# Kernel optimization log

Hardware: AMD Instinct MI355X
Metric: run time of the kernel (lower is better)

## Reference

```python
import jax, jax.numpy as jnp
import numpy as np

B, N, K = 4, 8192, 16
FEAT = 512
GRID = 45
M = GRID * GRID


def _p(key, shape, scale=0.05):
    return jax.random.normal(key, shape, dtype=jnp.float32) * scale


def setup_inputs() -> dict:
    key = jax.random.key(0)
    ks = jax.random.split(key, 40)
    inp = {"pts": jax.random.normal(ks[0], (B, N, 3), dtype=jnp.float32)}
    specs = {
        "w1": (64, 12), "b1": (64,), "w2": (64, 64), "b2": (64,), "w3": (64, 64), "b3": (64,),
        "g1a": (64, 64), "g1ab": (64,), "g1b": (128, 64), "g1bb": (128,),
        "g2a": (128, 128), "g2ab": (128,), "g2b": (1024, 128), "g2bb": (1024,),
        "m1": (FEAT, 1024), "m1b": (FEAT,), "m2": (FEAT, FEAT), "m2b": (FEAT,),
        "f1a": (FEAT, FEAT + 2), "f1ab": (FEAT,), "f1b": (FEAT, FEAT), "f1bb": (FEAT,), "f1c": (3, FEAT), "f1cb": (3,),
        "f2a": (FEAT, FEAT + 3), "f2ab": (FEAT,), "f2b": (FEAT, FEAT), "f2bb": (FEAT,), "f2c": (3, FEAT), "f2cb": (3,),
    }
    for i, (name, shp) in enumerate(specs.items()):
        inp[name] = _p(ks[i + 1], shp)
    return inp


def conv1x1(x, w, b):
    # x: (B,C,N), w: (Cout,Cin), b: (Cout,)
    return jnp.einsum('bcn,oc->bon', x, w) + b[None, :, None]


def knn_idx(x, k):
    # x: (B,C,N) -> neighbor indices (B,N,k) by smallest squared distance (self included)
    xt = jnp.swapaxes(x, 1, 2)                      # (B,N,C)
    sq = jnp.sum(xt * xt, axis=-1)                  # (B,N)
    inner = jnp.einsum('bnc,bmc->bnm', xt, xt)      # (B,N,N)
    neg_d2 = 2.0 * inner - sq[:, :, None] - sq[:, None, :]
    return jax.lax.top_k(neg_d2, k)[1]


def gather_nbrs(feats_t, idx):
    # feats_t: (B,N,C), idx: (B,N,k) -> (B,N,k,C)
    return jax.vmap(lambda f, i: f[i])(feats_t, idx)


def local_maxpool(x, idx):
    # x: (B,C,N) -> (B,C,N) max over k neighbors
    nb = gather_nbrs(jnp.swapaxes(x, 1, 2), idx)    # (B,N,k,C)
    return jnp.swapaxes(jnp.max(nb, axis=2), 1, 2)


def local_cov(pts_t, idx):
    # pts_t: (B,3,N) -> (B,12,N): coords + outer product of first two neighbors
    p = jnp.swapaxes(pts_t, 1, 2)                   # (B,N,3)
    nb = gather_nbrs(p, idx)                        # (B,N,k,3)
    outer = nb[:, :, 0, :, None] * nb[:, :, 1, None, :]   # (B,N,3,3)
    feat = jnp.concatenate([p, outer.reshape(p.shape[0], p.shape[1], 9)], axis=-1)
    return jnp.swapaxes(feat, 1, 2)


def _forward(pts, w1, b1, w2, b2, w3, b3, g1a, g1ab, g1b, g1bb, g2a, g2ab, g2b, g2bb,
             m1, m1b, m2, m2b, f1a, f1ab, f1b, f1bb, f1c, f1cb, f2a, f2ab, f2b, f2bb, f2c, f2cb):
    relu = jax.nn.relu
    pts_t = jnp.swapaxes(pts, 1, 2)                 # (B,3,N)
    # ---- encoder ----
    idx = knn_idx(pts_t, K)
    x = local_cov(pts_t, idx)                       # (B,12,N)
    x = relu(conv1x1(x, w1, b1))
    x = relu(conv1x1(x, w2, b2))
    x = relu(conv1x1(x, w3, b3))                    # (B,64,N)
    idx = knn_idx(x, K)
    g = local_maxpool(x, idx)
    g = conv1x1(relu(conv1x1(g, g1a, g1ab)), g1b, g1bb)   # (B,128,N)
    idx = knn_idx(g, K)
    h = local_maxpool(g, idx)
    h = conv1x1(relu(conv1x1(h, g2a, g2ab)), g2b, g2bb)   # (B,1024,N)
    glob = jnp.max(h, axis=2, keepdims=True)        # (B,1024,1)
    code = conv1x1(relu(conv1x1(glob, m1, m1b)), m2, m2b)  # (B,FEAT,1)
    # ---- decoder ----
    Bs = code.shape[0]
    cw = jnp.broadcast_to(code, (Bs, FEAT, M))
    lin = jnp.linspace(-0.3, 0.3, GRID, dtype=jnp.float32)
    gx, gy = jnp.meshgrid(lin, lin, indexing='ij')
    grid = jnp.stack([gx.ravel(), gy.ravel()], axis=0)     # (2,M)
    grid = jnp.broadcast_to(grid[None], (Bs, 2, M))

    def fold(points, wa, ba, wb, bb, wc, bc):
        y = jnp.concatenate([cw, points], axis=1)
        y = relu(conv1x1(y, wa, ba))
        y = relu(conv1x1(y, wb, bb))
        return conv1x1(y, wc, bc)                    # (B,3,M)

    mid = fold(grid, f1a, f1ab, f1b, f1bb, f1c, f1cb)
    rec = fold(mid, f2a, f2ab, f2b, f2bb, f2c, f2cb)
    return jnp.swapaxes(rec, 1, 2)                   # (B,M,3)


def reference(pts, w1, b1, w2, b2, w3, b3, g1a, g1ab, g1b, g1bb, g2a, g2ab, g2b, g2bb,
              m1, m1b, m2, m2b, f1a, f1ab, f1b, f1bb, f1c, f1cb, f2a, f2ab, f2b, f2bb, f2c, f2cb):
    return _forward(pts, w1, b1, w2, b2, w3, b3, g1a, g1ab, g1b, g1bb, g2a, g2ab, g2b, g2bb,
                    m1, m1b, m2, m2b, f1a, f1ab, f1b, f1bb, f1c, f1cb, f2a, f2ab, f2b, f2bb, f2c, f2cb)
```

## Files before the change

### kernel.cpp

```cpp
#include <hip/hip_runtime.h>
#include <stdint.h>

#define B_ 4
#define N_ 8192
#define K_ 16
#define FEAT_ 512
#define GRID_ 45
#define M_ (GRID_*GRID_)

typedef unsigned long long ull;
typedef __bf16 bf16x8 __attribute__((ext_vector_type(8)));
typedef float f32x16 __attribute__((ext_vector_type(16)));


__device__ __forceinline__ unsigned int fmap(float f){
  unsigned int u = __float_as_uint(f);
  return (u & 0x80000000u) ? ~u : (u | 0x80000000u);
}
__device__ __forceinline__ float funmap(unsigned int u){
  return (u & 0x80000000u) ? __uint_as_float(u ^ 0x80000000u) : __uint_as_float(~u);
}

__device__ __forceinline__ void ins16b(unsigned (&dk)[16], unsigned (&di)[16],
                                       unsigned k, unsigned id){
  if (k < dk[15]){
    bool c[16];
#pragma unroll
    for (int s = 0; s < 16; ++s) c[s] = k < dk[s];
#pragma unroll
    for (int s = 15; s >= 1; --s){
      dk[s] = c[s-1] ? dk[s-1] : (c[s] ? k  : dk[s]);
      di[s] = c[s-1] ? di[s-1] : (c[s] ? id : di[s]);
    }
    if (c[0]){ dk[0] = k; di[0] = id; }
  }
}

__device__ __forceinline__ void bsort16(ull (&c)[16]){
#pragma unroll
  for (int d = 8; d >= 1; d >>= 1){
#pragma unroll
    for (int i = 0; i < 16; ++i){
      if (!(i & d)){
        ull x = c[i], y = c[i|d];
        bool lt = x < y;
        c[i]   = lt ? x : y;
        c[i|d] = lt ? y : x;
      }
    }
  }
}
__device__ __forceinline__ void bmerge16(ull (&a)[16], const ull (&b)[16]){
#pragma unroll
  for (int i = 0; i < 16; ++i){
    ull bv = b[15-i];
    a[i] = a[i] < bv ? a[i] : bv;
  }
  bsort16(a);
}

__device__ __forceinline__ void bsplit(float x, unsigned short& h, unsigned short& l){
  __bf16 hh = (__bf16)x;
  __bf16 ll = (__bf16)(x - (float)hh);
  h = __builtin_bit_cast(unsigned short, hh);
  l = __builtin_bit_cast(unsigned short, ll);
}

#define GLDS16(l, g) __builtin_amdgcn_global_load_lds((const __attribute__((address_space(1))) void*)(g), (__attribute__((address_space(3))) void*)(l), 16, 0, 0)
#define GLDS4(l, g)  __builtin_amdgcn_global_load_lds((const __attribute__((address_space(1))) void*)(g), (__attribute__((address_space(3))) void*)(l), 4, 0, 0)

#define KEY_INF 0xFF800000FFFFFFFFull

__global__ void k_init(unsigned int* glob){
  int i = blockIdx.x*256 + threadIdx.x;
  if (i < B_*1024) glob[i] = 0x007FFFFFu;
}

__global__ __launch_bounds__(256) void k_nn1(const float* __restrict__ pts,
                                             unsigned long long* __restrict__ nn64){
  __shared__ __align__(16) float sp4[2048][4];
  int b = blockIdx.z, s = blockIdx.y;
  int c0 = s*2048;
  const float* P = pts + (size_t)b*N_*3;
  for (int p = threadIdx.x; p < 2048; p += 256){
    const float* src = P + (size_t)(c0 + p)*3;
    sp4[p][0] = src[0]; sp4[p][1] = src[1]; sp4[p][2] = src[2]; sp4[p][3] = 0.f;
  }
  __syncthreads();
  int n = blockIdx.x*256 + threadIdx.x;
  float qx = P[n*3], qy = P[n*3+1], qz = P[n*3+2];
  float best = 1e30f; int bi = 0;
  for (int j = 0; j < 2048; ++j){
    float4 sv = *(const float4*)sp4[j];
    float dx = qx - sv.x, dy = qy - sv.y, dz = qz - sv.z;
    float d2 = fmaf(dx,dx, fmaf(dy,dy, dz*dz));
    int cj = c0 + j;
    if (d2 < best && cj != n){ best = d2; bi = cj; }
  }
  unsigned long long key = ((unsigned long long)__float_as_uint(best) << 32) | (unsigned int)bi;
  atomicMin(&nn64[(size_t)b*N_ + n], key);
}

__global__ __launch_bounds__(256) void k_cov_mlp(const float* __restrict__ pts,
    const unsigned long long* __restrict__ nn64,
    const float* __restrict__ w1, const float* __restrict__ b1,
    const float* __restrict__ w2, const float* __restrict__ b2,
    const float* __restrict__ w3, const float* __restrict__ b3,
    float* __restrict__ xout, unsigned short* __restrict__ T,
    float* __restrict__ cc){
  __shared__ __align__(16) float W1t[12*64];
  __shared__ __align__(16) float W2t[64*64];
  __shared__ __align__(16) float W3t[64*64];
  __shared__ float B1[64], B2[64], B3[64];
  __shared__ __align__(16) float x0[64][12];
  __shared__ __align__(16) float h1[64][64];
  __shared__ __align__(16) float h2[64][64];
  int b = blockIdx.y; int n0 = blockIdx.x*64; int tid = threadIdx.x;
  for (int i = tid; i < 12*64; i += 256){ int o = i % 64, ci = i / 64; W1t[i] = w1[o*12 + ci]; }
  for (int i = tid; i < 64*64; i += 256){ int o = i % 64, ci = i / 64; W2t[i] = w2[o*64 + ci]; W3t[i] = w3[o*64 + ci]; }
  if (tid < 64){ B1[tid]=b1[tid]; B2[tid]=b2[tid]; B3[tid]=b3[tid]; }
  {
    int p = tid % 64, cg = tid / 64;
    int n = n0 + p;
    const float* P = pts + ((size_t)b*N_ + n)*3;
    int nb = (int)(nn64[(size_t)b*N_ + n] & 0xFFFFFFFFull);
    const float* Q = pts + ((size_t)b*N_ + nb)*3;
    if (cg == 0){ x0[p][0]=P[0]; x0[p][1]=P[1]; x0[p][2]=P[2]; }
    else { int i = cg-1; float pi = P[i];
      x0[p][3+i*3+0]=pi*Q[0]; x0[p][3+i*3+1]=pi*Q[1]; x0[p][3+i*3+2]=pi*Q[2]; }
  }
  __syncthreads();
  { int o = tid % 64, pg = tid / 64;
    for (int p = pg; p < 64; p += 4){
      float acc = B1[o];
#pragma unroll
      for (int ci = 0; ci < 12; ++ci) acc = fmaf(W1t[ci*64+o], x0[p][ci], acc);
      h1[p][o] = fmaxf(acc, 0.f);
    } }
  __syncthreads();
  { int o = tid % 64, pg = tid / 64;
    for (int p = pg; p < 64; p += 4){
      float acc = B2[o];
#pragma unroll
      for (int ci = 0; ci < 64; ++ci) acc = fmaf(W2t[ci*64+o], h1[p][ci], acc);
      h2[p][o] = fmaxf(acc, 0.f);
    } }
  __syncthreads();
  { int o = tid % 64, pg = tid / 64;
    for (int p = pg; p < 64; p += 4){
      float acc = B3[o];
#pragma unroll
      for (int ci = 0; ci < 64; ++ci) acc = fmaf(W3t[ci*64+o], h2[p][ci], acc);
      float r = fmaxf(acc, 0.f);
      xout[((size_t)b*N_ + n0 + p)*64 + o] = r;
      h1[p][o] = r;
    } }
  __syncthreads();
  {
    char* Tb = (char*)T;
    const size_t HS = (size_t)N_*16, PS = 2*HS, KS = 4*HS;
    const size_t Bb = (size_t)b*4*KS;
    for (int e = tid; e < 64*8; e += 256){
      int p = e >> 3, gg = e & 7;
      int kf = gg >> 1, h = gg & 1;
      unsigned short hs[8], ls[8];
#pragma unroll
      for (int j = 0; j < 8; ++j) bsplit(h1[p][gg*8+j], hs[j], ls[j]);
      size_t base = Bb + (size_t)kf*KS + (size_t)h*HS + (size_t)(n0+p)*16;
      *(uint4*)(Tb + base)      = *(uint4*)hs;
      *(uint4*)(Tb + base + PS) = *(uint4*)ls;
    }
    if (tid < 64){
      float ss = 0.f;
#pragma unroll 8
      for (int c = 0; c < 64; ++c){ float v = h1[tid][(c + tid) & 63]; ss = fmaf(v, v, ss); }
      cc[(size_t)b*N_ + n0 + tid] = ss;
    }
  }
}

template<int KF>
__global__ __launch_bounds__(256) void k_prep4(const float* __restrict__ f,
    unsigned short* __restrict__ T, float* __restrict__ cc){
  int b = blockIdx.y; int n = blockIdx.x*256 + threadIdx.x;
  const float* src = f + ((size_t)b*N_ + n)*(KF*16);
  char* Tb = (char*)T;
  float ss = 0.f;
#pragma unroll
  for (int kf = 0; kf < KF; ++kf){
    float v[16];
#pragma unroll
    for (int c4 = 0; c4 < 4; ++c4){
      float4 t4 = *(const float4*)&src[kf*16 + c4*4];
      v[c4*4]=t4.x; v[c4*4+1]=t4.y; v[c4*4+2]=t4.z; v[c4*4+3]=t4.w;
    }
    unsigned short hs[16], ls[16];
#pragma unroll
    for (int c = 0; c < 16; ++c){
      float x = v[c];
      ss = fmaf(x, x, ss);
      bsplit(x, hs[c], ls[c]);
    }
    size_t base = ((((size_t)b*KF + kf)*2)*2)*(size_t)(N_*16) + (size_t)n*16;
    const size_t HS = (size_t)N_*16;
    const size_t PS = 2*HS;
    *(uint4*)(Tb + base)            = *(uint4*)&hs[0];
    *(uint4*)(Tb + base + HS)       = *(uint4*)&hs[8];
    *(uint4*)(Tb + base + PS)       = *(uint4*)&ls[0];
    *(uint4*)(Tb + base + PS + HS)  = *(uint4*)&ls[8];
  }
  cc[(size_t)b*N_ + n] = ss;
}

template<int KF, int MW, int S>
__global__ __launch_bounds__(256, MW) void k_knnF(const unsigned short* __restrict__ T,
    const float* __restrict__ ccg, ull* __restrict__ qkeys){
  extern __shared__ char smem[];
  constexpr int NT = (N_/S)/64;
  char* As = smem;
  char* Cs = smem + KF*4096;

  const int tid = threadIdx.x, lane = tid & 63, wid = tid >> 6;
  const int hi = lane >> 5, l31 = lane & 31;
  const int b = blockIdx.z, sp = blockIdx.y, q0 = blockIdx.x*128;
  const int c0 = sp*(N_/S);
  const char* Tb = (const char*)T;
  const size_t HS = (size_t)N_*16, PS = 2*HS, KS = 4*HS;
  const size_t Bb = (size_t)b*KF*KS;
  const float* ccb = ccg + (size_t)b*N_;

  const int q = q0 + wid*32 + l31;
  bf16x8 qh[KF], ql[KF];
#pragma unroll
  for (int kf = 0; kf < KF; ++kf){
    size_t o = Bb + kf*KS + hi*HS + (size_t)q*16;
    qh[kf] = *(const bf16x8*)(Tb + o);
    ql[kf] = *(const bf16x8*)(Tb + o + PS);
  }

  unsigned dk[16], di[16];
#pragma unroll
  for (int t = 0; t < 16; ++t){ dk[t] = 0xFFFFFFFFu; di[t] = 0xFFFFFFFFu; }
  float kapf = __builtin_inff();

  auto stage = [&](int t0){
#pragma unroll
    for (int si = 0; si < KF; ++si){
      int s = wid + 4*si;
      int kf = s >> 2, pl = (s >> 1) & 1, h = s & 1;
      GLDS16(As + s*1024,
             Tb + Bb + kf*KS + pl*PS + h*HS + (size_t)(c0 + t0)*16);
    }
    if (wid == 0) GLDS4(Cs, (const char*)(ccb + c0 + t0));
  };

  for (int t = 0; t < NT; ++t){
    const int t0 = t*64;
    __syncthreads();
    stage(t0);
    asm volatile("s_waitcnt vmcnt(0)" ::: "memory");
    __syncthreads();

    const char* Ab = As + hi*1024 + l31*16;
    const float* cct = (const float*)Cs;
#pragma unroll
    for (int i = 0; i < 2; ++i){
      f32x16 acc = (f32x16)(0.f);
#pragma unroll
      for (int kf = 0; kf < KF; ++kf){
        bf16x8 ah = *(const bf16x8*)(Ab + kf*4096 + i*512);
        bf16x8 al = *(const bf16x8*)(Ab + kf*4096 + 2048 + i*512);
        acc = __builtin_amdgcn_mfma_f32_32x32x16_bf16(ah, qh[kf], acc, 0, 0, 0);
        acc = __builtin_amdgcn_mfma_f32_32x32x16_bf16(ah, ql[kf], acc, 0, 0, 0);
        acc = __builtin_amdgcn_mfma_f32_32x32x16_bf16(al, qh[kf], acc, 0, 0, 0);
      }
#pragma unroll
      for (int rq = 0; rq < 4; ++rq){
        float4 c4 = *(const float4*)(cct + i*32 + 4*hi + 8*rq);
        int rowb = c0 + t0 + i*32 + 4*hi + 8*rq;
        float v0 = fmaf(-2.f, acc[rq*4+0], c4.x);
        float v1 = fmaf(-2.f, acc[rq*4+1], c4.y);
        float v2 = fmaf(-2.f, acc[rq*4+2], c4.z);
        float v3 = fmaf(-2.f, acc[rq*4+3], c4.w);
        if (fminf(fminf(v0, v1), fminf(v2, v3)) < kapf){
          if (v0 < kapf) ins16b(dk, di, fmap(v0), (unsigned)(rowb+0));
          if (v1 < kapf) ins16b(dk, di, fmap(v1), (unsigned)(rowb+1));
          if (v2 < kapf) ins16b(dk, di, fmap(v2), (unsigned)(rowb+2));
          if (v3 < kapf) ins16b(dk, di, fmap(v3), (unsigned)(rowb+3));
          unsigned kk = dk[15];
          kapf = (kk >= 0xFF800000u) ? __builtin_inff() : funmap(kk);
        }
      }
    }
  }
  ull* op = qkeys + (((size_t)((size_t)b*N_ + q)*S + sp)*2 + hi)*16;
#pragma unroll
  for (int t = 0; t < 16; ++t) op[t] = ((ull)dk[t] << 32) | di[t];
}

template<int S>
__global__ void k_sel(const ull* __restrict__ qkeys, int* __restrict__ idxout){
  int i = blockIdx.x*256 + threadIdx.x;
  if (i >= B_*N_) return;
  const ull* kp = qkeys + (size_t)i*(S*32);
  ull a[16], t[16];
#pragma unroll
  for (int u = 0; u < 16; ++u) a[u] = kp[u];
#pragma unroll
  for (int r = 1; r < S*2; ++r){
#pragma unroll
    for (int u = 0; u < 16; ++u) t[u] = kp[r*16 + u];
    bmerge16(a, t);
  }
  int* op = idxout + (size_t)i*16;
#pragma unroll
  for (int u = 0; u < 16; ++u) op[u] = (int)(a[u] & 0xffffffffu);
}

__global__ __launch_bounds__(256) void k_gpool_mlp(const float* __restrict__ x,
    const int* __restrict__ idx,
    const float* __restrict__ g1a, const float* __restrict__ g1ab,
    const float* __restrict__ g1b, const float* __restrict__ g1bb,
    float* __restrict__ gout){
  __shared__ __align__(16) float Wt1[64*64];
  __shared__ __align__(16) float Wt2[64*128];
  __shared__ float Ba[64], Bb[128];
  __shared__ __align__(16) float m[64][64];
  __shared__ __align__(16) float r[64][64];
  int b = blockIdx.y; int n0 = blockIdx.x*64; int tid = threadIdx.x;
  for (int i = tid; i < 64*64; i += 256){ int o = i%64, ci = i/64; Wt1[i] = g1a[o*64+ci]; }
  for (int i = tid; i < 64*128; i += 256){ int o = i%128, ci = i/128; Wt2[i] = g1b[o*64+ci]; }
  if (tid < 64) Ba[tid] = g1ab[tid];
  if (tid < 128) Bb[tid] = g1bb[tid];
  { int p = tid/4, cg = tid%4; int n = n0 + p;
    const int* ip = idx + ((size_t)b*N_ + n)*16;
    float mm[16];
#pragma unroll
    for (int u = 0; u < 16; ++u) mm[u] = -1e30f;
    for (int k = 0; k < 16; ++k){
      int nb = ip[k];
      const float4* src = (const float4*)(x + ((size_t)b*N_ + nb)*64 + cg*16);
#pragma unroll
      for (int u = 0; u < 4; ++u){
        float4 v = src[u];
        mm[4*u  ] = fmaxf(mm[4*u  ], v.x); mm[4*u+1] = fmaxf(mm[4*u+1], v.y);
        mm[4*u+2] = fmaxf(mm[4*u+2], v.z); mm[4*u+3] = fmaxf(mm[4*u+3], v.w);
      }
    }
#pragma unroll
    for (int u = 0; u < 16; ++u) m[p][cg*16+u] = mm[u];
  }
  __syncthreads();
  { int o = tid%64, pg = tid/64;
    float acc[16];
#pragma unroll
    for (int u = 0; u < 16; ++u) acc[u] = Ba[o];
    for (int ci = 0; ci < 64; ci += 4){
      float w0 = Wt1[ci*64+o], w1_ = Wt1[(ci+1)*64+o], w2_ = Wt1[(ci+2)*64+o], w3_ = Wt1[(ci+3)*64+o];
#pragma unroll
      for (int u = 0; u < 16; ++u){
        float4 mv = *(const float4*)&m[pg*16+u][ci];
        acc[u] = fmaf(w0, mv.x, acc[u]); acc[u] = fmaf(w1_, mv.y, acc[u]);
        acc[u] = fmaf(w2_, mv.z, acc[u]); acc[u] = fmaf(w3_, mv.w, acc[u]);
      }
    }
#pragma unroll
    for (int u = 0; u < 16; ++u) r[pg*16+u][o] = fmaxf(acc[u], 0.f);
  }
  __syncthreads();
  { int o = tid%128, pg = tid/128;
    float acc[32];
#pragma unroll
    for (int u = 0; u < 32; ++u) acc[u] = Bb[o];
    for (int ci = 0; ci < 64; ci += 4){
      float w0 = Wt2[ci*128+o], w1_ = Wt2[(ci+1)*128+o], w2_ = Wt2[(ci+2)*128+o], w3_ = Wt2[(ci+3)*128+o];
#pragma unroll
      for (int u = 0; u < 32; ++u){
        float4 rv = *(const float4*)&r[pg*32+u][ci];
        acc[u] = fmaf(w0, rv.x, acc[u]); acc[u] = fmaf(w1_, rv.y, acc[u]);
        acc[u] = fmaf(w2_, rv.z, acc[u]); acc[u] = fmaf(w3_, rv.w, acc[u]);
      }
    }
#pragma unroll
    for (int u = 0; u < 32; ++u)
      gout[((size_t)b*N_ + n0 + pg*32 + u)*128 + o] = acc[u];
  }
}

__global__ __launch_bounds__(256) void k_hpool_max(const float* __restrict__ g,
    const int* __restrict__ idx,
    const float* __restrict__ g2a, const float* __restrict__ g2ab,
    const float* __restrict__ g2b, const float* __restrict__ g2bb,
    unsigned int* __restrict__ glob){
  __shared__ __align__(16) float m[32][128];
  __shared__ __align__(16) float t[32][128];
  int b = blockIdx.y; int n0 = blockIdx.x*32; int tid = threadIdx.x;
  { int p = tid/8, cg = tid%8; int n = n0+p;
    const int* ip = idx + ((size_t)b*N_+n)*16;
    float mm[16];
#pragma unroll
    for (int u = 0; u < 16; ++u) mm[u] = -1e30f;
    for (int k = 0; k < 16; ++k){
      int nb = ip[k];
      const float4* src = (const float4*)(g + ((size_t)b*N_+nb)*128 + cg*16);
#pragma unroll
      for (int u = 0; u < 4; ++u){
        float4 v = src[u];
        mm[4*u  ] = fmaxf(mm[4*u  ], v.x); mm[4*u+1] = fmaxf(mm[4*u+1], v.y);
        mm[4*u+2] = fmaxf(mm[4*u+2], v.z); mm[4*u+3] = fmaxf(mm[4*u+3], v.w);
      }
    }
#pragma unroll
    for (int u = 0; u < 16; ++u) m[p][cg*16+u] = mm[u];
  }
  __syncthreads();
  { int o = tid%128, pg = tid/128;
    float acc[16];
#pragma unroll
    for (int u = 0; u < 16; ++u) acc[u] = g2ab[o];
    const float4* wrow = (const float4*)(g2a + (size_t)o*128);
    for (int c4 = 0; c4 < 32; ++c4){
      float4 wv = wrow[c4];
#pragma unroll
      for (int u = 0; u < 16; ++u){
        float4 mv = *(const float4*)&m[pg*16+u][c4*4];
        acc[u] = fmaf(wv.x,mv.x,acc[u]); acc[u] = fmaf(wv.y,mv.y,acc[u]);
        acc[u] = fmaf(wv.z,mv.z,acc[u]); acc[u] = fmaf(wv.w,mv.w,acc[u]);
      }
    }
#pragma unroll
    for (int u = 0; u < 16; ++u) t[pg*16+u][o] = fmaxf(acc[u], 0.f);
  }
  __syncthreads();
  for (int op = 0; op < 2; ++op){
    int o0 = op*512 + tid;
    const float4* wr0 = (const float4*)(g2b + (size_t)o0*128);
    const float4* wr1 = (const float4*)(g2b + (size_t)(o0+256)*128);
    float a0[32], a1[32];
#pragma unroll
    for (int u = 0; u < 32; ++u){ a0[u] = 0.f; a1[u] = 0.f; }
    for (int c4 = 0; c4 < 32; ++c4){
      float4 w0 = wr0[c4], w1 = wr1[c4];
#pragma unroll
      for (int u = 0; u < 32; ++u){
        float4 tv = *(const float4*)&t[u][c4*4];
        a0[u] = fmaf(w0.x,tv.x,a0[u]); a0[u] = fmaf(w0.y,tv.y,a0[u]);
        a0[u] = fmaf(w0.z,tv.z,a0[u]); a0[u] = fmaf(w0.w,tv.w,a0[u]);
        a1[u] = fmaf(w1.x,tv.x,a1[u]); a1[u] = fmaf(w1.y,tv.y,a1[u]);
        a1[u] = fmaf(w1.z,tv.z,a1[u]); a1[u] = fmaf(w1.w,tv.w,a1[u]);
      }
    }
    float b0 = g2bb[o0], b1 = g2bb[o0+256];
    float mx0 = -1e30f, mx1 = -1e30f;
#pragma unroll
    for (int u = 0; u < 32; ++u){
      mx0 = fmaxf(mx0, a0[u] + b0);
      mx1 = fmaxf(mx1, a1[u] + b1);
    }
    atomicMax(&glob[b*1024 + o0],       fmap(mx0));
    atomicMax(&glob[b*1024 + o0 + 256], fmap(mx1));
  }
}

__global__ __launch_bounds__(512) void k_code(const unsigned int* __restrict__ glob,
    const float* __restrict__ m1, const float* __restrict__ m1b,
    const float* __restrict__ m2, const float* __restrict__ m2b,
    const float* __restrict__ f1a, const float* __restrict__ f1ab,
    const float* __restrict__ f2a, const float* __restrict__ f2ab,
    float* __restrict__ base1, float* __restrict__ base2){
  __shared__ __align__(16) float gl_s[1024];
  __shared__ __align__(16) float hid_s[512];
  __shared__ __align__(16) float code_s[512];
  int b = blockIdx.x; int tid = threadIdx.x;
  for (int i = tid; i < 1024; i += 512) gl_s[i] = funmap(glob[b*1024+i]);
  __syncthreads();
  { float acc = m1b[tid];
    const float4* wr = (const float4*)(m1 + (size_t)tid*1024);
    for (int c4 = 0; c4 < 256; ++c4){ float4 wv = wr[c4]; float4 gv = *(const float4*)&gl_s[c4*4];
      acc = fmaf(wv.x,gv.x,acc); acc = fmaf(wv.y,gv.y,acc);
      acc = fmaf(wv.z,gv.z,acc); acc = fmaf(wv.w,gv.w,acc); }
    hid_s[tid] = fmaxf(acc, 0.f);
  }
  __syncthreads();
  { float acc = m2b[tid];
    const float4* wr = (const float4*)(m2 + (size_t)tid*512);
    for (int c4 = 0; c4 < 128; ++c4){ float4 wv = wr[c4]; float4 hv = *(const float4*)&hid_s[c4*4];
      acc = fmaf(wv.x,hv.x,acc); acc = fmaf(wv.y,hv.y,acc);
      acc = fmaf(wv.z,hv.z,acc); acc = fmaf(wv.w,hv.w,acc); }
    code_s[tid] = acc;
  }
  __syncthreads();
  { float acc = f1ab[tid];
    const float* wr = f1a + (size_t)tid*514;
    for (int c = 0; c < 512; ++c) acc = fmaf(wr[c], code_s[c], acc);
    base1[b*512 + tid] = acc;
  }
  { float acc = f2ab[tid];
    const float* wr = f2a + (size_t)tid*515;
    for (int c = 0; c < 512; ++c) acc = fmaf(wr[c], code_s[c], acc);
    base2[b*512 + tid] = acc;
  }
}

template<int NIN>
__global__ __launch_bounds__(256) void k_fold(const float* __restrict__ base,
    const float* __restrict__ fa,
    const float* __restrict__ fb, const float* __restrict__ fbb,
    const float* __restrict__ fc, const float* __restrict__ fcb,
    const float* __restrict__ pin, float* __restrict__ pout){
  __shared__ __align__(16) float y1[16][512];
  __shared__ __align__(16) float y2[16][516];
  __shared__ float pcoord[16][NIN];
  int b = blockIdx.y; int m0 = blockIdx.x*16; int tid = threadIdx.x;
  if (tid < 16*NIN){
    int p = tid / NIN, c = tid % NIN;
    int mm = min(m0 + p, M_-1);
    float v;
    if (NIN == 2){
      const float step = 0.6f/44.f;
      int ii = (c == 0) ? (mm/GRID_) : (mm%GRID_);
      v = -0.3f + step*ii;
    } else {
      v = pin[((size_t)b*M_ + mm)*3 + c];
    }
    pcoord[p][c] = v;
  }
  __syncthreads();
  const int stride_a = 512 + NIN;
  for (int rep = 0; rep < 2; ++rep){
    int o = rep*256 + tid;
    float av[NIN];
#pragma unroll
    for (int c = 0; c < NIN; ++c) av[c] = fa[(size_t)o*stride_a + 512 + c];
    float bv = base[b*512 + o];
#pragma unroll
    for (int p = 0; p < 16; ++p){
      float acc = bv;
#pragma unroll
      for (int c = 0; c < NIN; ++c) acc = fmaf(av[c], pcoord[p][c], acc);
      y1[p][o] = fmaxf(acc, 0.f);
    }
  }
  __syncthreads();
  {
    const float* wr0 = fb + (size_t)tid*512;
    const float* wr1 = fb + (size_t)(tid+256)*512;
    float a0[16], a1[16];
#pragma unroll
    for (int u = 0; u < 16; ++u){ a0[u] = 0.f; a1[u] = 0.f; }
    for (int c4 = 0; c4 < 128; ++c4){
      float4 w0 = *(const float4*)&wr0[c4*4];
      float4 w1 = *(const float4*)&wr1[c4*4];
#pragma unroll
      for (int u = 0; u < 16; ++u){
        float4 yv = *(const float4*)&y1[u][c4*4];
        a0[u] = fmaf(w0.x,yv.x,a0[u]); a0[u] = fmaf(w0.y,yv.y,a0[u]);
        a0[u] = fmaf(w0.z,yv.z,a0[u]); a0[u] = fmaf(w0.w,yv.w,a0[u]);
        a1[u] = fmaf(w1.x,yv.x,a1[u]); a1[u] = fmaf(w1.y,yv.y,a1[u]);
        a1[u] = fmaf(w1.z,yv.z,a1[u]); a1[u] = fmaf(w1.w,yv.w,a1[u]);
      }
    }
    float b0 = fbb[tid], b1 = fbb[tid+256];
#pragma unroll
    for (int u = 0; u < 16; ++u){
      y2[u][tid]     = fmaxf(a0[u] + b0, 0.f);
      y2[u][tid+256] = fmaxf(a1[u] + b1, 0.f);
    }
  }
  __syncthreads();
  if (tid < 48){
    int p = tid / 3, c = tid % 3;
    const float* wr = fc + (size_t)c*512;
    float acc = fcb[c];
    for (int o4 = 0; o4 < 128; ++o4){
      float4 wv = *(const float4*)&wr[o4*4];
      float4 yv = *(const float4*)&y2[p][o4*4];
      acc = fmaf(wv.x,yv.x,acc); acc = fmaf(wv.y,yv.y,acc);
      acc = fmaf(wv.z,yv.z,acc); acc = fmaf(wv.w,yv.w,acc);
    }
    int mm = m0 + p;
    if (mm < M_) pout[((size_t)b*M_ + mm)*3 + c] = acc;
  }
}

extern "C" void kernel_launch(void* const* d_in, const int* in_sizes, int n_in,
                              void* d_out, int out_size, void* d_ws, size_t ws_size,
                              hipStream_t stream){
  const float* pts  = (const float*)d_in[0];
  const float* w1   = (const float*)d_in[1];  const float* b1   = (const float*)d_in[2];
  const float* w2   = (const float*)d_in[3];  const float* b2   = (const float*)d_in[4];
  const float* w3   = (const float*)d_in[5];  const float* b3   = (const float*)d_in[6];
  const float* g1a  = (const float*)d_in[7];  const float* g1ab = (const float*)d_in[8];
  const float* g1b  = (const float*)d_in[9];  const float* g1bb = (const float*)d_in[10];
  const float* g2a  = (const float*)d_in[11]; const float* g2ab = (const float*)d_in[12];
  const float* g2b  = (const float*)d_in[13]; const float* g2bb = (const float*)d_in[14];
  const float* m1   = (const float*)d_in[15]; const float* m1b  = (const float*)d_in[16];
  const float* m2   = (const float*)d_in[17]; const float* m2b  = (const float*)d_in[18];
  const float* f1a  = (const float*)d_in[19]; const float* f1ab = (const float*)d_in[20];
  const float* f1b  = (const float*)d_in[21]; const float* f1bb = (const float*)d_in[22];
  const float* f1c  = (const float*)d_in[23]; const float* f1cb = (const float*)d_in[24];
  const float* f2a  = (const float*)d_in[25]; const float* f2ab = (const float*)d_in[26];
  const float* f2b  = (const float*)d_in[27]; const float* f2bb = (const float*)d_in[28];
  const float* f2c  = (const float*)d_in[29]; const float* f2cb = (const float*)d_in[30];
  float* out = (float*)d_out;

  char* w = (char*)d_ws;
  auto alloc = [&](size_t bytes){ char* p = w; w += (bytes + 255) & ~(size_t)255; return p; };
  unsigned long long* nn64 = (unsigned long long*)alloc((size_t)B_*N_*8);
  float* x    = (float*)alloc((size_t)B_*N_*64*4);
  float* g    = (float*)alloc((size_t)B_*N_*128*4);
  unsigned short* T64  = (unsigned short*)alloc((size_t)B_*4*4*N_*16);
  unsigned short* T128 = (unsigned short*)alloc((size_t)B_*8*4*N_*16);
  float* ccf  = (float*)alloc((size_t)B_*N_*4);
  int*   idx  = (int*)alloc((size_t)B_*N_*16*4);
  ull*   qkeys = (ull*)alloc((size_t)B_*N_*4*2*16*8);
  unsigned int* glob = (unsigned int*)alloc((size_t)B_*1024*4);
  float* base1 = (float*)alloc((size_t)B_*512*4);
  float* base2 = (float*)alloc((size_t)B_*512*4);
  float* mid   = (float*)alloc((size_t)B_*M_*3*4);
  (void)ws_size; (void)in_sizes; (void)n_in; (void)out_size;

  const int SMEM4 = 4*4096 + 256;
  const int SMEM8 = 8*4096 + 256;
  hipFuncSetAttribute((const void*)k_knnF<4,2,2>, hipFuncAttributeMaxDynamicSharedMemorySize, SMEM4);
  hipFuncSetAttribute((const void*)k_knnF<8,2,2>, hipFuncAttributeMaxDynamicSharedMemorySize, SMEM8);

  hipMemsetAsync(nn64, 0xFF, (size_t)B_*N_*8, stream);
  k_init<<<dim3((B_*1024+255)/256), 256, 0, stream>>>(glob);
  k_nn1<<<dim3(N_/256, 4, B_), 256, 0, stream>>>(pts, nn64);
  k_cov_mlp<<<dim3(N_/64, B_), 256, 0, stream>>>(pts, nn64, w1,b1,w2,b2,w3,b3, x, T64, ccf);

  k_knnF<4,2,2><<<dim3(N_/128, 2, B_), 256, SMEM4, stream>>>(T64, ccf, qkeys);
  k_sel<2><<<dim3(B_*N_/256), 256, 0, stream>>>(qkeys, idx);

  k_gpool_mlp<<<dim3(N_/64, B_), 256, 0, stream>>>(x, idx, g1a,g1ab,g1b,g1bb, g);

  k_prep4<8><<<dim3(N_/256, B_), 256, 0, stream>>>(g, T128, ccf);
  k_knnF<8,2,2><<<dim3(N_/128, 2, B_), 256, SMEM8, stream>>>(T128, ccf, qkeys);
  k_sel<2><<<dim3(B_*N_/256), 256, 0, stream>>>(qkeys, idx);

  k_hpool_max<<<dim3(N_/32, B_), 256, 0, stream>>>(g, idx, g2a,g2ab,g2b,g2bb, glob);
  k_code<<<dim3(B_), 512, 0, stream>>>(glob, m1,m1b,m2,m2b, f1a,f1ab, f2a,f2ab, base1, base2);
  k_fold<2><<<dim3((M_+15)/16, B_), 256, 0, stream>>>(base1, f1a, f1b, f1bb, f1c, f1cb, nullptr, mid);
  k_fold<3><<<dim3((M_+15)/16, B_), 256, 0, stream>>>(base2, f2a, f2b, f2bb, f2c, f2cb, mid, out);
}
```

Measured before the change: 1.567 ms.

## Register-tile small MLP layers and split kNN across more column partitions

```diff
diff --git a/kernel.cpp b/kernel.cpp
--- a/kernel.cpp
+++ b/kernel.cpp
@@ -138,23 +138,56 @@
       h1[p][o] = fmaxf(acc, 0.f);
     } }
   __syncthreads();
-  { int o = tid % 64, pg = tid / 64;
-    for (int p = pg; p < 64; p += 4){
-      float acc = B2[o];
-#pragma unroll
-      for (int ci = 0; ci < 64; ++ci) acc = fmaf(W2t[ci*64+o], h1[p][ci], acc);
-      h2[p][o] = fmaxf(acc, 0.f);
-    } }
-  __syncthreads();
-  { int o = tid % 64, pg = tid / 64;
-    for (int p = pg; p < 64; p += 4){
-      float acc = B3[o];
-#pragma unroll
-      for (int ci = 0; ci < 64; ++ci) acc = fmaf(W3t[ci*64+o], h2[p][ci], acc);
-      float r = fmaxf(acc, 0.f);
-      xout[((size_t)b*N_ + n0 + p)*64 + o] = r;
-      h1[p][o] = r;
-    } }
+  {
+    int o = tid & 31, pg = tid >> 5;
+    float a0[8], a1[8];
+#pragma unroll
+    for (int u = 0; u < 8; ++u){ a0[u] = B2[o]; a1[u] = B2[o+32]; }
+    for (int ci = 0; ci < 64; ci += 4){
+      float w00=W2t[ci*64+o],      w01=W2t[(ci+1)*64+o],      w02=W2t[(ci+2)*64+o],      w03=W2t[(ci+3)*64+o];
+      float w10=W2t[ci*64+o+32],   w11=W2t[(ci+1)*64+o+32],   w12=W2t[(ci+2)*64+o+32],   w13=W2t[(ci+3)*64+o+32];
+#pragma unroll
+      for (int u = 0; u < 8; ++u){
+        float4 hv = *(const float4*)&h1[pg*8+u][ci];
+        a0[u] = fmaf(w00,hv.x,a0[u]); a0[u] = fmaf(w01,hv.y,a0[u]);
+        a0[u] = fmaf(w02,hv.z,a0[u]); a0[u] = fmaf(w03,hv.w,a0[u]);
+        a1[u] = fmaf(w10,hv.x,a1[u]); a1[u] = fmaf(w11,hv.y,a1[u]);
+        a1[u] = fmaf(w12,hv.z,a1[u]); a1[u] = fmaf(w13,hv.w,a1[u]);
+      }
+    }
+#pragma unroll
+    for (int u = 0; u < 8; ++u){
+      h2[pg*8+u][o]    = fmaxf(a0[u], 0.f);
+      h2[pg*8+u][o+32] = fmaxf(a1[u], 0.f);
+    }
+  }
+  __syncthreads();
+  {
+    int o = tid & 31, pg = tid >> 5;
+    float a0[8], a1[8];
+#pragma unroll
+    for (int u = 0; u < 8; ++u){ a0[u] = B3[o]; a1[u] = B3[o+32]; }
+    for (int ci = 0; ci < 64; ci += 4){
+      float w00=W3t[ci*64+o],      w01=W3t[(ci+1)*64+o],      w02=W3t[(ci+2)*64+o],      w03=W3t[(ci+3)*64+o];
+      float w10=W3t[ci*64+o+32],   w11=W3t[(ci+1)*64+o+32],   w12=W3t[(ci+2)*64+o+32],   w13=W3t[(ci+3)*64+o+32];
+#pragma unroll
+      for (int u = 0; u < 8; ++u){
+        float4 hv = *(const float4*)&h2[pg*8+u][ci];
+        a0[u] = fmaf(w00,hv.x,a0[u]); a0[u] = fmaf(w01,hv.y,a0[u]);
+        a0[u] = fmaf(w02,hv.z,a0[u]); a0[u] = fmaf(w03,hv.w,a0[u]);
+        a1[u] = fmaf(w10,hv.x,a1[u]); a1[u] = fmaf(w11,hv.y,a1[u]);
+        a1[u] = fmaf(w12,hv.z,a1[u]); a1[u] = fmaf(w13,hv.w,a1[u]);
+      }
+    }
+#pragma unroll
+    for (int u = 0; u < 8; ++u){
+      int p = pg*8 + u;
+      float r0 = fmaxf(a0[u], 0.f), r1 = fmaxf(a1[u], 0.f);
+      xout[((size_t)b*N_ + n0 + p)*64 + o]      = r0;
+      xout[((size_t)b*N_ + n0 + p)*64 + o + 32] = r1;
+      h1[p][o] = r0; h1[p][o+32] = r1;
+    }
+  }
   __syncthreads();
   {
     char* Tb = (char*)T;
@@ -351,39 +384,52 @@
     for (int u = 0; u < 16; ++u) m[p][cg*16+u] = mm[u];
   }
   __syncthreads();
-  { int o = tid%64, pg = tid/64;
-    float acc[16];
-#pragma unroll
-    for (int u = 0; u < 16; ++u) acc[u] = Ba[o];
+  {
+    int o = tid & 31, pg = tid >> 5;
+    float a0[8], a1[8];
+#pragma unroll
+    for (int u = 0; u < 8; ++u){ a0[u] = Ba[o]; a1[u] = Ba[o+32]; }
     for (int ci = 0; ci < 64; ci += 4){
-      float w0 = Wt1[ci*64+o], w1_ = Wt1[(ci+1)*64+o], w2_ = Wt1[(ci+2)*64+o], w3_ = Wt1[(ci+3)*64+o];
+      float w00=Wt1[ci*64+o],      w01=Wt1[(ci+1)*64+o],      w02=Wt1[(ci+2)*64+o],      w03=Wt1[(ci+3)*64+o];
+      float w10=Wt1[ci*64+o+32],   w11=Wt1[(ci+1)*64+o+32],   w12=Wt1[(ci+2)*64+o+32],   w13=Wt1[(ci+3)*64+o+32];
+#pragma unroll
+      for (int u = 0; u < 8; ++u){
+        float4 mv = *(const float4*)&m[pg*8+u][ci];
+        a0[u] = fmaf(w00,mv.x,a0[u]); a0[u] = fmaf(w01,mv.y,a0[u]);
+        a0[u] = fmaf(w02,mv.z,a0[u]); a0[u] = fmaf(w03,mv.w,a0[u]);
+        a1[u] = fmaf(w10,mv.x,a1[u]); a1[u] = fmaf(w11,mv.y,a1[u]);
+        a1[u] = fmaf(w12,mv.z,a1[u]); a1[u] = fmaf(w13,mv.w,a1[u]);
+      }
+    }
+#pragma unroll
+    for (int u = 0; u < 8; ++u){
+      r[pg*8+u][o]    = fmaxf(a0[u], 0.f);
+      r[pg*8+u][o+32] = fmaxf(a1[u], 0.f);
+    }
+  }
+  __syncthreads();
+  {
+    int o = tid & 63, pg = tid >> 6;
+    float a0[16], a1[16];
+#pragma unroll
+    for (int u = 0; u < 16; ++u){ a0[u] = Bb[o]; a1[u] = Bb[o+64]; }
+    for (int ci = 0; ci < 64; ci += 4){
+      float w00=Wt2[ci*128+o],      w01=Wt2[(ci+1)*128+o],      w02=Wt2[(ci+2)*128+o],      w03=Wt2[(ci+3)*128+o];
+      float w10=Wt2[ci*128+o+64],   w11=Wt2[(ci+1)*128+o+64],   w12=Wt2[(ci+2)*128+o+64],   w13=Wt2[(ci+3)*128+o+64];
 #pragma unroll
       for (int u = 0; u < 16; ++u){
-        float4 mv = *(const float4*)&m[pg*16+u][ci];
-        acc[u] = fmaf(w0, mv.x, acc[u]); acc[u] = fmaf(w1_, mv.y, acc[u]);
-        acc[u] = fmaf(w2_, mv.z, acc[u]); acc[u] = fmaf(w3_, mv.w, acc[u]);
-      }
-    }
-#pragma unroll
-    for (int u = 0; u < 16; ++u) r[pg*16+u][o] = fmaxf(acc[u], 0.f);
-  }
-  __syncthreads();
-  { int o = tid%128, pg = tid/128;
-    float acc[32];
-#pragma unroll
-    for (int u = 0; u < 32; ++u) acc[u] = Bb[o];
-    for (int ci = 0; ci < 64; ci += 4){
-      float w0 = Wt2[ci*128+o], w1_ = Wt2[(ci+1)*128+o], w2_ = Wt2[(ci+2)*128+o], w3_ = Wt2[(ci+3)*128+o];
-#pragma unroll
-      for (int u = 0; u < 32; ++u){
-        float4 rv = *(const float4*)&r[pg*32+u][ci];
-        acc[u] = fmaf(w0, rv.x, acc[u]); acc[u] = fmaf(w1_, rv.y, acc[u]);
-        acc[u] = fmaf(w2_, rv.z, acc[u]); acc[u] = fmaf(w3_, rv.w, acc[u]);
-      }
-    }
-#pragma unroll
-    for (int u = 0; u < 32; ++u)
-      gout[((size_t)b*N_ + n0 + pg*32 + u)*128 + o] = acc[u];
+        float4 rv = *(const float4*)&r[pg*16+u][ci];
+        a0[u] = fmaf(w00,rv.x,a0[u]); a0[u] = fmaf(w01,rv.y,a0[u]);
+        a0[u] = fmaf(w02,rv.z,a0[u]); a0[u] = fmaf(w03,rv.w,a0[u]);
+        a1[u] = fmaf(w10,rv.x,a1[u]); a1[u] = fmaf(w11,rv.y,a1[u]);
+        a1[u] = fmaf(w12,rv.z,a1[u]); a1[u] = fmaf(w13,rv.w,a1[u]);
+      }
+    }
+#pragma unroll
+    for (int u = 0; u < 16; ++u){
+      gout[((size_t)b*N_ + n0 + pg*16 + u)*128 + o]      = a0[u];
+      gout[((size_t)b*N_ + n0 + pg*16 + u)*128 + o + 64] = a1[u];
+    }
   }
 }
 
@@ -622,22 +668,22 @@
 
   const int SMEM4 = 4*4096 + 256;
   const int SMEM8 = 8*4096 + 256;
-  hipFuncSetAttribute((const void*)k_knnF<4,2,2>, hipFuncAttributeMaxDynamicSharedMemorySize, SMEM4);
-  hipFuncSetAttribute((const void*)k_knnF<8,2,2>, hipFuncAttributeMaxDynamicSharedMemorySize, SMEM8);
+  hipFuncSetAttribute((const void*)k_knnF<4,4,4>, hipFuncAttributeMaxDynamicSharedMemorySize, SMEM4);
+  hipFuncSetAttribute((const void*)k_knnF<8,3,4>, hipFuncAttributeMaxDynamicSharedMemorySize, SMEM8);
 
   hipMemsetAsync(nn64, 0xFF, (size_t)B_*N_*8, stream);
   k_init<<<dim3((B_*1024+255)/256), 256, 0, stream>>>(glob);
   k_nn1<<<dim3(N_/256, 4, B_), 256, 0, stream>>>(pts, nn64);
   k_cov_mlp<<<dim3(N_/64, B_), 256, 0, stream>>>(pts, nn64, w1,b1,w2,b2,w3,b3, x, T64, ccf);
 
-  k_knnF<4,2,2><<<dim3(N_/128, 2, B_), 256, SMEM4, stream>>>(T64, ccf, qkeys);
-  k_sel<2><<<dim3(B_*N_/256), 256, 0, stream>>>(qkeys, idx);
+  k_knnF<4,4,4><<<dim3(N_/128, 4, B_), 256, SMEM4, stream>>>(T64, ccf, qkeys);
+  k_sel<4><<<dim3(B_*N_/256), 256, 0, stream>>>(qkeys, idx);
 
   k_gpool_mlp<<<dim3(N_/64, B_), 256, 0, stream>>>(x, idx, g1a,g1ab,g1b,g1bb, g);
 
   k_prep4<8><<<dim3(N_/256, B_), 256, 0, stream>>>(g, T128, ccf);
-  k_knnF<8,2,2><<<dim3(N_/128, 2, B_), 256, SMEM8, stream>>>(T128, ccf, qkeys);
-  k_sel<2><<<dim3(B_*N_/256), 256, 0, stream>>>(qkeys, idx);
+  k_knnF<8,3,4><<<dim3(N_/128, 4, B_), 256, SMEM8, stream>>>(T128, ccf, qkeys);
+  k_sel<4><<<dim3(B_*N_/256), 256, 0, stream>>>(qkeys, idx);
 
   k_hpool_max<<<dim3(N_/32, B_), 256, 0, stream>>>(g, idx, g2a,g2ab,g2b,g2bb, glob);
   k_code<<<dim3(B_), 512, 0, stream>>>(glob, m1,m1b,m2,m2b, f1a,f1ab, f2a,f2ab, base1, base2);
```

After: 1.501 ms, median of 2. 4.2% less time.
